# Kernel optimization log

Hardware: AMD Instinct MI355X
Metric: run time of the kernel (lower is better)

## Reference

```python
import jax, jax.numpy as jnp
import numpy as np
import math

DIM = 512
BLOCK_NUM = 16
SEQ_LEN = 8192
BLOCK_LEN = SEQ_LEN // BLOCK_NUM  # 512 == DIM -> mask used as-is
BATCH = 4
LN_EPS = 1e-3  # keras LayerNormalization default epsilon


def setup_inputs() -> dict:
    key = jax.random.key(0)
    ks = jax.random.split(key, 5)
    inputs = jax.random.normal(ks[0], (BATCH, BLOCK_NUM, BLOCK_LEN, DIM), dtype=jnp.float32)
    # binary padding-style mask, values in {0,1}
    mask_array = jax.random.randint(ks[1], (BATCH, SEQ_LEN, DIM), 0, 2).astype(jnp.float32)
    scale = 1.0 / math.sqrt(DIM)
    dw1 = jax.random.normal(ks[2], (DIM, DIM), dtype=jnp.float32) * scale
    dw2 = jax.random.normal(ks[3], (DIM, DIM), dtype=jnp.float32) * scale
    dw3 = jax.random.normal(ks[4], (DIM, DIM), dtype=jnp.float32) * scale
    db1 = jnp.zeros((DIM,), dtype=jnp.float32)
    db2 = jnp.zeros((DIM,), dtype=jnp.float32)
    db3 = jnp.zeros((DIM,), dtype=jnp.float32)
    return {"inputs": inputs, "mask_array": mask_array,
            "dw1": dw1, "dw2": dw2, "dw3": dw3,
            "db1": db1, "db2": db2, "db3": db3}


def reference(inputs, mask_array, dw1, dw2, dw3, db1, db2, db3):
    # inputs: [B, block_num, block_len, dim]
    Q = jnp.matmul(inputs, dw1) + db1
    K = jnp.matmul(inputs, dw2) + db2
    V = jnpp_matmul = jnp.matmul(inputs, dw3) + db3
    V = jnp.matmul(inputs, dw3) + db3
    # block-local attention scores: [B, bn, bl, bl]
    scores = jnp.einsum('bnqd,bnkd->bnqk', Q, K) / math.sqrt(DIM)
    # mask: [B, seq_len, dim] -> [B, bn, bl, dim]; block_len == dim so no slice/tile
    m = mask_array.reshape(BATCH, BLOCK_NUM, BLOCK_LEN, DIM)
    scores = scores + (1.0 - m) * jnp.float32(-1e10)
    p = jax.nn.softmax(scores, axis=-1)
    out = jnp.einsum('bnqk,bnkd->bnqd', p, V) + inputs  # residual
    # LayerNorm(axis=-1), fresh keras layer: gamma=1, beta=0, eps=1e-3
    mean = jnp.mean(out, axis=-1, keepdims=True)
    var = jnp.mean(jnp.square(out - mean), axis=-1, keepdims=True)
    return (out - mean) / jnp.sqrt(var + LN_EPS)
```

## Files before the change

kernel.cpp:

```cpp
#include <hip/hip_runtime.h>

#define DIMK 512
#define NBLK 64
#define NTOK 32768

typedef short  short8 __attribute__((ext_vector_type(8)));
typedef float  f32x4  __attribute__((ext_vector_type(4)));
typedef unsigned short u16x8 __attribute__((ext_vector_type(8)));

__device__ __forceinline__ unsigned short f2bf(float f) {
  union { float f; unsigned u; } v; v.f = f;
  unsigned r = (v.u + 0x7FFFu + ((v.u >> 16) & 1u)) >> 16;
  return (unsigned short)r;
}
__device__ __forceinline__ float bf2f(unsigned short h) {
  return __uint_as_float(((unsigned)h) << 16);
}

__device__ __forceinline__ void gload_lds16(const unsigned short* g,
                                            unsigned short* l) {
  __builtin_amdgcn_global_load_lds(
      (const __attribute__((address_space(1))) unsigned int*)(g),
      (__attribute__((address_space(3))) unsigned int*)(l),
      16, 0, 0);
}


__global__ __launch_bounds__(256) void k_wt_prep(
    const float* __restrict__ dw1, const float* __restrict__ dw2,
    const float* __restrict__ dw3, unsigned short* __restrict__ Wt)
{
  __shared__ float t[64][65];
  const int b = blockIdx.x;
  const int w = b >> 6;
  const int tt = b & 63;
  const int kt = (tt >> 3) * 64;
  const int nt = (tt & 7) * 64;
  const float* dw = (w == 0) ? dw1 : (w == 1) ? dw2 : dw3;
  const int tid = threadIdx.x;
  const int rr = tid >> 4;
  const int cc = (tid & 15) << 2;

#pragma unroll
  for (int p = 0; p < 4; ++p) {
    const int r = rr + p * 16;
    const float4 v = *(const float4*)&dw[(size_t)(kt + r) * 512 + nt + cc];
    t[cc + 0][r] = v.x; t[cc + 1][r] = v.y;
    t[cc + 2][r] = v.z; t[cc + 3][r] = v.w;
  }
  __syncthreads();
#pragma unroll
  for (int p = 0; p < 4; ++p) {
    const int r = rr + p * 16;
    const int n = nt + r;
    const int k = kt + cc;
    ushort4 o;
    o.x = f2bf(t[r][cc + 0]); o.y = f2bf(t[r][cc + 1]);
    o.z = f2bf(t[r][cc + 2]); o.w = f2bf(t[r][cc + 3]);
    *(ushort4*)&Wt[(size_t)w * 262144 + (size_t)(k >> 5) * 16384 +
                   (size_t)n * 32 + (k & 31)] = o;
  }
}

__global__ __launch_bounds__(256) void k_xconv(
    const float* __restrict__ X, unsigned short* __restrict__ Xb)
{
  const size_t gid = (size_t)blockIdx.x * 256 + threadIdx.x;
  const size_t i = gid * 8;
  const int tok = (int)(i >> 9);
  const int col = (int)(i & 511);
  const float4 a = *(const float4*)(X + i);
  const float4 b = *(const float4*)(X + i + 4);
  u16x8 o;
  o[0] = f2bf(a.x); o[1] = f2bf(a.y); o[2] = f2bf(a.z); o[3] = f2bf(a.w);
  o[4] = f2bf(b.x); o[5] = f2bf(b.y); o[6] = f2bf(b.z); o[7] = f2bf(b.w);
  *(u16x8*)(Xb + ((size_t)(tok >> 7) * 16 + (col >> 5)) * 4096 +
            (tok & 127) * 32 + (col & 31)) = o;
}

__global__ __launch_bounds__(256) void k_bitpack(
    const float* __restrict__ mask, unsigned char* __restrict__ bits)
{
  const size_t gid = (size_t)blockIdx.x * 256 + threadIdx.x;
  const size_t i = gid * 8;
  const float4 ma = *(const float4*)(mask + i);
  const float4 mb = *(const float4*)(mask + i + 4);
  unsigned v = 0;
  v |= (ma.x > 0.5f) << 0; v |= (ma.y > 0.5f) << 1;
  v |= (ma.z > 0.5f) << 2; v |= (ma.w > 0.5f) << 3;
  v |= (mb.x > 0.5f) << 4; v |= (mb.y > 0.5f) << 5;
  v |= (mb.z > 0.5f) << 6; v |= (mb.w > 0.5f) << 7;
  bits[gid] = (unsigned char)v;
}

__global__ __launch_bounds__(256, 2) void k_qkv(
    const unsigned short* __restrict__ Xb, const unsigned short* __restrict__ Wt,
    const float* __restrict__ db1, const float* __restrict__ db2,
    const float* __restrict__ db3,
    unsigned short* __restrict__ Qb, unsigned short* __restrict__ Kb,
    unsigned short* __restrict__ Vt)
{
  __shared__ __align__(16) unsigned short smem[32768];

  const int id = blockIdx.x;
  const int x = id & 7, j = id >> 3;
  const int mtile = x * 32 + (j >> 2);
  const int nt = j & 3;
  const int m0 = mtile * 128;
  const int n0 = nt * 128;

  const int tid = threadIdx.x, lane = tid & 63, wv = tid >> 6;
  const int quad = lane >> 4, l16 = lane & 15;
  const int rb = (wv >> 1) * 64, cb = (wv & 1) * 64;

  f32x4 acc[3][4][4];
#pragma unroll
  for (int w = 0; w < 3; ++w)
#pragma unroll
    for (int i = 0; i < 4; ++i)
#pragma unroll
      for (int jj = 0; jj < 4; ++jj) {
        f32x4 z = {0.f, 0.f, 0.f, 0.f}; acc[w][i][jj] = z;
      }

  auto stage = [&](unsigned short* base, int it) {
    const unsigned short* aslab = Xb + ((size_t)mtile * 16 + it) * 4096;
    gload_lds16(aslab + tid * 8, base + tid * 8);
    gload_lds16(aslab + (tid + 256) * 8, base + (tid + 256) * 8);
#pragma unroll
    for (int h = 0; h < 6; ++h) {
      const int c = tid + h * 256;
      const int w = c >> 9, cc = c & 511;
      const unsigned short* bslab =
          Wt + (size_t)w * 262144 + (size_t)it * 16384 + (size_t)n0 * 32;
      gload_lds16(bslab + cc * 8, base + 4096 + w * 4096 + cc * 8);
    }
  };

  stage(smem, 0);
  __syncthreads();
  int cur = 0;
  for (int it = 0; it < 16; ++it) {
    unsigned short* cbuf = smem + cur * 16384;
    if (it < 15) stage(smem + (cur ^ 1) * 16384, it + 1);
    const unsigned short* As = cbuf;
    const unsigned short* Bs = cbuf + 4096;
    short8 af[4];
#pragma unroll
    for (int i = 0; i < 4; ++i)
      af[i] = *(const short8*)&As[(rb + i * 16 + l16) * 32 + quad * 8];
#pragma unroll
    for (int jj = 0; jj < 4; ++jj)
#pragma unroll
      for (int w = 0; w < 3; ++w) {
        const short8 bf =
            *(const short8*)&Bs[w * 4096 + (cb + jj * 16 + l16) * 32 + quad * 8];
#pragma unroll
        for (int i = 0; i < 4; ++i)
          acc[w][i][jj] = __builtin_amdgcn_mfma_f32_16x16x32_bf16(
              af[i], bf, acc[w][i][jj], 0, 0, 0);
      }
    __syncthreads();
    cur ^= 1;
  }

#pragma unroll
  for (int i = 0; i < 4; ++i)
#pragma unroll
    for (int jj = 0; jj < 4; ++jj)
#pragma unroll
      for (int r = 0; r < 4; ++r) {
        const int tok = m0 + rb + i * 16 + quad * 4 + r;
        const int col = n0 + cb + jj * 16 + l16;
        Qb[((size_t)(tok >> 6) * 16 + (col >> 5)) * 2048 +
           (tok & 63) * 32 + (col & 31)] = f2bf(acc[0][i][jj][r] + db1[col]);
        Kb[((size_t)(tok >> 9) * 16 + (col >> 5)) * 16384 +
           (tok & 511) * 32 + (col & 31)] = f2bf(acc[1][i][jj][r] + db2[col]);
      }
#pragma unroll
  for (int i = 0; i < 4; ++i)
#pragma unroll
    for (int jj = 0; jj < 4; ++jj) {
      const int cl = cb + jj * 16 + l16;
      const int t0 = rb + i * 16 + quad * 4;
      const float bv = db3[n0 + cl];
      ushort4 pk;
      pk.x = f2bf(acc[2][i][jj][0] + bv);
      pk.y = f2bf(acc[2][i][jj][1] + bv);
      pk.z = f2bf(acc[2][i][jj][2] + bv);
      pk.w = f2bf(acc[2][i][jj][3] + bv);
      *(ushort4*)&smem[cl * 136 + t0] = pk;
    }
  __syncthreads();
#pragma unroll
  for (int h = 0; h < 8; ++h) {
    const int c = tid + h * 256;
    const int cl = c >> 4, toff = (c & 15) * 8;
    const int tg = mtile * 128 + toff;
    *(u16x8*)&Vt[(size_t)(tg >> 5) * 16384 + (size_t)(n0 + cl) * 32 +
                 (tg & 31)] = *(const u16x8*)&smem[cl * 136 + toff];
  }
}

__global__ __launch_bounds__(256, 2) void k_attn_p(
    const unsigned short* __restrict__ Qb, const unsigned short* __restrict__ Kb,
    const unsigned long long* __restrict__ bits, unsigned short* __restrict__ Pb)
{
  __shared__ __align__(16) unsigned short smem[36864];
  __shared__ float red[4][64];
  const int tid = threadIdx.x, lane = tid & 63, wv = tid >> 6;
  const int quad = lane >> 4, l16 = lane & 15;
  const int blk = blockIdx.x & 63, mt = blockIdx.x >> 6;
  const size_t q0 = (size_t)blk * 512 + (size_t)mt * 64;
  const int qt = blk * 8 + mt;

  f32x4 acc[4][8];
#pragma unroll
  for (int i = 0; i < 4; ++i)
#pragma unroll
    for (int j = 0; j < 8; ++j) { f32x4 z = {0.f, 0.f, 0.f, 0.f}; acc[i][j] = z; }

  auto stage = [&](unsigned short* base, int it) {
    const unsigned short* aslab = Qb + ((size_t)qt * 16 + it) * 2048;
    gload_lds16(aslab + tid * 8, base + tid * 8);
    const unsigned short* bslab = Kb + ((size_t)blk * 16 + it) * 16384;
#pragma unroll
    for (int h = 0; h < 8; ++h) {
      const int c = tid + h * 256;
      gload_lds16(bslab + c * 8, base + 2048 + c * 8);
    }
  };

  stage(smem, 0);
  __syncthreads();
  int cur = 0;
  for (int it = 0; it < 16; ++it) {
    unsigned short* cbuf = smem + cur * 18432;
    if (it < 15) stage(smem + (cur ^ 1) * 18432, it + 1);
    const unsigned short* As = cbuf;
    const unsigned short* Bs = cbuf + 2048;
    short8 af[4], bfv[8];
#pragma unroll
    for (int i = 0; i < 4; ++i)
      af[i] = *(const short8*)&As[(i * 16 + l16) * 32 + quad * 8];
#pragma unroll
    for (int j = 0; j < 8; ++j)
      bfv[j] = *(const short8*)&Bs[(wv * 128 + j * 16 + l16) * 32 + quad * 8];
#pragma unroll
    for (int i = 0; i < 4; ++i)
#pragma unroll
      for (int j = 0; j < 8; ++j)
        acc[i][j] = __builtin_amdgcn_mfma_f32_16x16x32_bf16(
            af[i], bfv[j], acc[i][j], 0, 0, 0);
    __syncthreads();
    cur ^= 1;
  }

  const float scale = 0.04419417382415922f;
  float rmax[4][4];
#pragma unroll
  for (int i = 0; i < 4; ++i)
#pragma unroll
    for (int r = 0; r < 4; ++r) rmax[i][r] = -3.0e38f;
#pragma unroll
  for (int i = 0; i < 4; ++i)
#pragma unroll
    for (int r = 0; r < 4; ++r) {
      const size_t tok = q0 + i * 16 + quad * 4 + r;
      const unsigned long long w0 = bits[tok * 8 + wv * 2];
      const unsigned long long w1 = bits[tok * 8 + wv * 2 + 1];
#pragma unroll
      for (int j = 0; j < 8; ++j) {
        const unsigned long long sel = (j < 4) ? w0 : w1;
        const float bias = ((sel >> (l16 + 16 * (j & 3))) & 1ull) ? 0.0f : -1e10f;
        const float v = acc[i][j][r] * scale + bias;
        acc[i][j][r] = v;
        rmax[i][r] = fmaxf(rmax[i][r], v);
      }
    }
#pragma unroll
  for (int i = 0; i < 4; ++i)
#pragma unroll
    for (int r = 0; r < 4; ++r)
      for (int d = 1; d < 16; d <<= 1)
        rmax[i][r] = fmaxf(rmax[i][r], __shfl_xor(rmax[i][r], d, 64));
  if (l16 == 0)
#pragma unroll
    for (int i = 0; i < 4; ++i)
#pragma unroll
      for (int r = 0; r < 4; ++r) red[wv][i * 16 + quad * 4 + r] = rmax[i][r];
  __syncthreads();
#pragma unroll
  for (int i = 0; i < 4; ++i)
#pragma unroll
    for (int r = 0; r < 4; ++r) {
      const int row = i * 16 + quad * 4 + r;
      rmax[i][r] = fmaxf(fmaxf(red[0][row], red[1][row]),
                         fmaxf(red[2][row], red[3][row]));
    }
  __syncthreads();
  float rsum[4][4];
#pragma unroll
  for (int i = 0; i < 4; ++i)
#pragma unroll
    for (int r = 0; r < 4; ++r) rsum[i][r] = 0.f;
#pragma unroll
  for (int i = 0; i < 4; ++i)
#pragma unroll
    for (int j = 0; j < 8; ++j)
#pragma unroll
      for (int r = 0; r < 4; ++r) {
        const float e = __expf(acc[i][j][r] - rmax[i][r]);
        acc[i][j][r] = e;
        rsum[i][r] += e;
      }
#pragma unroll
  for (int i = 0; i < 4; ++i)
#pragma unroll
    for (int r = 0; r < 4; ++r)
      for (int d = 1; d < 16; d <<= 1)
        rsum[i][r] += __shfl_xor(rsum[i][r], d, 64);
  if (l16 == 0)
#pragma unroll
    for (int i = 0; i < 4; ++i)
#pragma unroll
      for (int r = 0; r < 4; ++r) red[wv][i * 16 + quad * 4 + r] = rsum[i][r];
  __syncthreads();
#pragma unroll
  for (int i = 0; i < 4; ++i)
#pragma unroll
    for (int r = 0; r < 4; ++r) {
      const int row = i * 16 + quad * 4 + r;
      rsum[i][r] = 1.0f / (red[0][row] + red[1][row] + red[2][row] + red[3][row]);
    }
#pragma unroll
  for (int i = 0; i < 4; ++i)
#pragma unroll
    for (int j = 0; j < 8; ++j)
#pragma unroll
      for (int r = 0; r < 4; ++r) {
        const int tok = (int)(q0 + i * 16 + quad * 4 + r);
        const int col = wv * 128 + j * 16 + l16;
        Pb[((size_t)(tok >> 6) * 16 + (col >> 5)) * 2048 +
           (tok & 63) * 32 + (col & 31)] = f2bf(acc[i][j][r] * rsum[i][r]);
      }
}

__global__ __launch_bounds__(256, 2) void k_pv_ln(
    const unsigned short* __restrict__ Pb, const unsigned short* __restrict__ Vt,
    const unsigned short* __restrict__ Xb, float* __restrict__ Out)
{
  __shared__ __align__(16) unsigned short smem[36864];
  __shared__ float2 red[4][64];
  const int tid = threadIdx.x, lane = tid & 63, wv = tid >> 6;
  const int quad = lane >> 4, l16 = lane & 15;
  const int blk = blockIdx.x & 63, mt = blockIdx.x >> 6;
  const size_t q0 = (size_t)blk * 512 + (size_t)mt * 64;
  const int qt = blk * 8 + mt;

  f32x4 acc[4][8];
#pragma unroll
  for (int i = 0; i < 4; ++i)
#pragma unroll
    for (int j = 0; j < 8; ++j) { f32x4 z = {0.f, 0.f, 0.f, 0.f}; acc[i][j] = z; }

  auto stage = [&](unsigned short* base, int it) {
    const unsigned short* aslab = Pb + ((size_t)qt * 16 + it) * 2048;
    gload_lds16(aslab + tid * 8, base + tid * 8);
    const unsigned short* bslab = Vt + ((size_t)blk * 16 + it) * 16384;
#pragma unroll
    for (int h = 0; h < 8; ++h) {
      const int c = tid + h * 256;
      gload_lds16(bslab + c * 8, base + 2048 + c * 8);
    }
  };

  stage(smem, 0);
  __syncthreads();
  int cur = 0;
  for (int it = 0; it < 16; ++it) {
    unsigned short* cbuf = smem + cur * 18432;
    if (it < 15) stage(smem + (cur ^ 1) * 18432, it + 1);
    const unsigned short* As = cbuf;
    const unsigned short* Bs = cbuf + 2048;
    short8 af[4], bfv[8];
#pragma unroll
    for (int i = 0; i < 4; ++i)
      af[i] = *(const short8*)&As[(i * 16 + l16) * 32 + quad * 8];
#pragma unroll
    for (int j = 0; j < 8; ++j)
      bfv[j] = *(const short8*)&Bs[(wv * 128 + j * 16 + l16) * 32 + quad * 8];
#pragma unroll
    for (int i = 0; i < 4; ++i)
#pragma unroll
      for (int j = 0; j < 8; ++j)
        acc[i][j] = __builtin_amdgcn_mfma_f32_16x16x32_bf16(
            af[i], bfv[j], acc[i][j], 0, 0, 0);
    __syncthreads();
    cur ^= 1;
  }

  float vsum[4][4], vsq[4][4];
#pragma unroll
  for (int i = 0; i < 4; ++i)
#pragma unroll
    for (int r = 0; r < 4; ++r) { vsum[i][r] = 0.f; vsq[i][r] = 0.f; }
#pragma unroll
  for (int i = 0; i < 4; ++i)
#pragma unroll
    for (int j = 0; j < 8; ++j)
#pragma unroll
      for (int r = 0; r < 4; ++r) {
        const int tok = (int)(q0 + i * 16 + quad * 4 + r);
        const int col = wv * 128 + j * 16 + l16;
        const float v = acc[i][j][r] +
            bf2f(Xb[((size_t)(tok >> 7) * 16 + (col >> 5)) * 4096 +
                    (tok & 127) * 32 + (col & 31)]);
        acc[i][j][r] = v;
        vsum[i][r] += v;
        vsq[i][r] += v * v;
      }
#pragma unroll
  for (int i = 0; i < 4; ++i)
#pragma unroll
    for (int r = 0; r < 4; ++r)
      for (int d = 1; d < 16; d <<= 1) {
        vsum[i][r] += __shfl_xor(vsum[i][r], d, 64);
        vsq[i][r]  += __shfl_xor(vsq[i][r], d, 64);
      }
  if (l16 == 0)
#pragma unroll
    for (int i = 0; i < 4; ++i)
#pragma unroll
      for (int r = 0; r < 4; ++r) {
        float2 p; p.x = vsum[i][r]; p.y = vsq[i][r];
        red[wv][i * 16 + quad * 4 + r] = p;
      }
  __syncthreads();
#pragma unroll
  for (int i = 0; i < 4; ++i)
#pragma unroll
    for (int r = 0; r < 4; ++r) {
      const int row = i * 16 + quad * 4 + r;
      float s = 0.f, q = 0.f;
#pragma unroll
      for (int w = 0; w < 4; ++w) { s += red[w][row].x; q += red[w][row].y; }
      const float mean = s * (1.0f / 512.0f);
      const float var  = q * (1.0f / 512.0f) - mean * mean;
      vsum[i][r] = mean;
      vsq[i][r]  = rsqrtf(var + 1e-3f);
    }
#pragma unroll
  for (int i = 0; i < 4; ++i)
#pragma unroll
    for (int j = 0; j < 8; ++j)
#pragma unroll
      for (int r = 0; r < 4; ++r) {
        const size_t tok = q0 + i * 16 + quad * 4 + r;
        const int col = wv * 128 + j * 16 + l16;
        Out[tok * (size_t)DIMK + col] =
            (acc[i][j][r] - vsum[i][r]) * vsq[i][r];
      }
}

extern "C" void kernel_launch(void* const* d_in, const int* in_sizes, int n_in,
                              void* d_out, int out_size, void* d_ws, size_t ws_size,
                              hipStream_t stream)
{
  const float* X    = (const float*)d_in[0];
  const float* mask = (const float*)d_in[1];
  const float* dw1  = (const float*)d_in[2];
  const float* dw2  = (const float*)d_in[3];
  const float* dw3  = (const float*)d_in[4];
  const float* db1  = (const float*)d_in[5];
  const float* db2  = (const float*)d_in[6];
  const float* db3  = (const float*)d_in[7];
  float* Out = (float*)d_out;

  char* ws = (char*)d_ws;
  const size_t MB = 1ull << 20;
  unsigned short* Wt = (unsigned short*)(ws);
  unsigned short* Qb = (unsigned short*)(ws + 2 * MB);
  unsigned short* Kb = (unsigned short*)(ws + 34 * MB);
  unsigned short* Vt = (unsigned short*)(ws + 66 * MB);
  unsigned short* Xb = (unsigned short*)(ws + 98 * MB);
  unsigned short* Pb = Qb;
  unsigned char*  bits = (unsigned char*)d_out;

  k_wt_prep<<<192, 256, 0, stream>>>(dw1, dw2, dw3, Wt);
  k_xconv  <<<8192, 256, 0, stream>>>(X, Xb);
  k_bitpack<<<8192, 256, 0, stream>>>(mask, bits);
  k_qkv    <<<1024, 256, 0, stream>>>(Xb, Wt, db1, db2, db3, Qb, Kb, Vt);
  k_attn_p <<<512, 256, 0, stream>>>(Qb, Kb, (const unsigned long long*)bits, Pb);
  k_pv_ln  <<<512, 256, 0, stream>>>(Pb, Vt, Xb, Out);
}
```

Baseline: 302.8 us.

## Triple-buffer GEMM loops, swizzle LDS layout, and merge prep kernels

The three GEMM-style kernels move from double to triple buffering. Each iteration now waits with an explicit vmcnt so loads run two stages ahead and the per-iteration __syncthreads calls are gone. The global-to-LDS copies use an XOR swizzle on 16-byte chunks, with matching swizzled fragment reads, to cut LDS bank conflicts. Launch bounds drop to one block per CU to make room for the larger LDS footprint, and the three preprocessing kernels are merged into one launch. The larger LDS use lowers occupancy, and the hard-coded vmcnt values depend on how many loads each stage issues.

```diff
diff --git a/kernel.cpp b/kernel.cpp
--- a/kernel.cpp
+++ b/kernel.cpp
@@ -25,82 +25,81 @@
       16, 0, 0);
 }
 
-
-__global__ __launch_bounds__(256) void k_wt_prep(
+__device__ __forceinline__ int swz(int c) { return c ^ ((c >> 3) & 3); }
+
+
+__global__ __launch_bounds__(256) void k_prep(
+    const float* __restrict__ X, const float* __restrict__ mask,
     const float* __restrict__ dw1, const float* __restrict__ dw2,
-    const float* __restrict__ dw3, unsigned short* __restrict__ Wt)
+    const float* __restrict__ dw3,
+    unsigned short* __restrict__ Xb, unsigned char* __restrict__ bits,
+    unsigned short* __restrict__ Wt)
 {
   __shared__ float t[64][65];
   const int b = blockIdx.x;
-  const int w = b >> 6;
-  const int tt = b & 63;
-  const int kt = (tt >> 3) * 64;
-  const int nt = (tt & 7) * 64;
-  const float* dw = (w == 0) ? dw1 : (w == 1) ? dw2 : dw3;
   const int tid = threadIdx.x;
-  const int rr = tid >> 4;
-  const int cc = (tid & 15) << 2;
-
-#pragma unroll
-  for (int p = 0; p < 4; ++p) {
-    const int r = rr + p * 16;
-    const float4 v = *(const float4*)&dw[(size_t)(kt + r) * 512 + nt + cc];
-    t[cc + 0][r] = v.x; t[cc + 1][r] = v.y;
-    t[cc + 2][r] = v.z; t[cc + 3][r] = v.w;
+  if (b < 8192) {
+    const size_t gid = (size_t)b * 256 + tid;
+    const size_t i = gid * 8;
+    const int tok = (int)(i >> 9);
+    const int col = (int)(i & 511);
+    const float4 a = *(const float4*)(X + i);
+    const float4 bb = *(const float4*)(X + i + 4);
+    u16x8 o;
+    o[0] = f2bf(a.x); o[1] = f2bf(a.y); o[2] = f2bf(a.z); o[3] = f2bf(a.w);
+    o[4] = f2bf(bb.x); o[5] = f2bf(bb.y); o[6] = f2bf(bb.z); o[7] = f2bf(bb.w);
+    *(u16x8*)(Xb + ((size_t)(tok >> 7) * 16 + (col >> 5)) * 4096 +
+              (tok & 127) * 32 + (col & 31)) = o;
+  } else if (b < 16384) {
+    const size_t gid = (size_t)(b - 8192) * 256 + tid;
+    const size_t i = gid * 8;
+    const float4 ma = *(const float4*)(mask + i);
+    const float4 mb = *(const float4*)(mask + i + 4);
+    unsigned v = 0;
+    v |= (ma.x > 0.5f) << 0; v |= (ma.y > 0.5f) << 1;
+    v |= (ma.z > 0.5f) << 2; v |= (ma.w > 0.5f) << 3;
+    v |= (mb.x > 0.5f) << 4; v |= (mb.y > 0.5f) << 5;
+    v |= (mb.z > 0.5f) << 6; v |= (mb.w > 0.5f) << 7;
+    bits[gid] = (unsigned char)v;
+  } else {
+    const int bb = b - 16384;
+    const int w = bb >> 6;
+    const int tt = bb & 63;
+    const int kt = (tt >> 3) * 64;
+    const int nt = (tt & 7) * 64;
+    const float* dw = (w == 0) ? dw1 : (w == 1) ? dw2 : dw3;
+    const int rr = tid >> 4;
+    const int cc = (tid & 15) << 2;
+#pragma unroll
+    for (int p = 0; p < 4; ++p) {
+      const int r = rr + p * 16;
+      const float4 v = *(const float4*)&dw[(size_t)(kt + r) * 512 + nt + cc];
+      t[cc + 0][r] = v.x; t[cc + 1][r] = v.y;
+      t[cc + 2][r] = v.z; t[cc + 3][r] = v.w;
+    }
+    __syncthreads();
+#pragma unroll
+    for (int p = 0; p < 4; ++p) {
+      const int r = rr + p * 16;
+      const int n = nt + r;
+      const int k = kt + cc;
+      ushort4 o;
+      o.x = f2bf(t[r][cc + 0]); o.y = f2bf(t[r][cc + 1]);
+      o.z = f2bf(t[r][cc + 2]); o.w = f2bf(t[r][cc + 3]);
+      *(ushort4*)&Wt[(size_t)w * 262144 + (size_t)(k >> 5) * 16384 +
+                     (size_t)n * 32 + (k & 31)] = o;
+    }
   }
-  __syncthreads();
-#pragma unroll
-  for (int p = 0; p < 4; ++p) {
-    const int r = rr + p * 16;
-    const int n = nt + r;
-    const int k = kt + cc;
-    ushort4 o;
-    o.x = f2bf(t[r][cc + 0]); o.y = f2bf(t[r][cc + 1]);
-    o.z = f2bf(t[r][cc + 2]); o.w = f2bf(t[r][cc + 3]);
-    *(ushort4*)&Wt[(size_t)w * 262144 + (size_t)(k >> 5) * 16384 +
-                   (size_t)n * 32 + (k & 31)] = o;
-  }
-}
-
-__global__ __launch_bounds__(256) void k_xconv(
-    const float* __restrict__ X, unsigned short* __restrict__ Xb)
-{
-  const size_t gid = (size_t)blockIdx.x * 256 + threadIdx.x;
-  const size_t i = gid * 8;
-  const int tok = (int)(i >> 9);
-  const int col = (int)(i & 511);
-  const float4 a = *(const float4*)(X + i);
-  const float4 b = *(const float4*)(X + i + 4);
-  u16x8 o;
-  o[0] = f2bf(a.x); o[1] = f2bf(a.y); o[2] = f2bf(a.z); o[3] = f2bf(a.w);
-  o[4] = f2bf(b.x); o[5] = f2bf(b.y); o[6] = f2bf(b.z); o[7] = f2bf(b.w);
-  *(u16x8*)(Xb + ((size_t)(tok >> 7) * 16 + (col >> 5)) * 4096 +
-            (tok & 127) * 32 + (col & 31)) = o;
-}
-
-__global__ __launch_bounds__(256) void k_bitpack(
-    const float* __restrict__ mask, unsigned char* __restrict__ bits)
-{
-  const size_t gid = (size_t)blockIdx.x * 256 + threadIdx.x;
-  const size_t i = gid * 8;
-  const float4 ma = *(const float4*)(mask + i);
-  const float4 mb = *(const float4*)(mask + i + 4);
-  unsigned v = 0;
-  v |= (ma.x > 0.5f) << 0; v |= (ma.y > 0.5f) << 1;
-  v |= (ma.z > 0.5f) << 2; v |= (ma.w > 0.5f) << 3;
-  v |= (mb.x > 0.5f) << 4; v |= (mb.y > 0.5f) << 5;
-  v |= (mb.z > 0.5f) << 6; v |= (mb.w > 0.5f) << 7;
-  bits[gid] = (unsigned char)v;
-}
-
-__global__ __launch_bounds__(256, 2) void k_qkv(
+}
+
+__global__ __launch_bounds__(256, 1) void k_qkv(
     const unsigned short* __restrict__ Xb, const unsigned short* __restrict__ Wt,
     const float* __restrict__ db1, const float* __restrict__ db2,
     const float* __restrict__ db3,
     unsigned short* __restrict__ Qb, unsigned short* __restrict__ Kb,
     unsigned short* __restrict__ Vt)
 {
-  __shared__ __align__(16) unsigned short smem[32768];
+  __shared__ __align__(16) unsigned short smem[49152];
 
   const int id = blockIdx.x;
   const int x = id & 7, j = id >> 3;
@@ -111,6 +110,7 @@
 
   const int tid = threadIdx.x, lane = tid & 63, wv = tid >> 6;
   const int quad = lane >> 4, l16 = lane & 15;
+  const int qx = quad ^ ((l16 >> 1) & 3);
   const int rb = (wv >> 1) * 64, cb = (wv & 1) * 64;
 
   f32x4 acc[3][4][4];
@@ -123,46 +123,48 @@
         f32x4 z = {0.f, 0.f, 0.f, 0.f}; acc[w][i][jj] = z;
       }
 
-  auto stage = [&](unsigned short* base, int it) {
+  auto stage = [&](int it) {
+    unsigned short* base = smem + (it % 3) * 16384;
     const unsigned short* aslab = Xb + ((size_t)mtile * 16 + it) * 4096;
-    gload_lds16(aslab + tid * 8, base + tid * 8);
-    gload_lds16(aslab + (tid + 256) * 8, base + (tid + 256) * 8);
+    gload_lds16(aslab + swz(tid) * 8, base + tid * 8);
+    gload_lds16(aslab + swz(tid + 256) * 8, base + (tid + 256) * 8);
 #pragma unroll
     for (int h = 0; h < 6; ++h) {
       const int c = tid + h * 256;
       const int w = c >> 9, cc = c & 511;
       const unsigned short* bslab =
           Wt + (size_t)w * 262144 + (size_t)it * 16384 + (size_t)n0 * 32;
-      gload_lds16(bslab + cc * 8, base + 4096 + w * 4096 + cc * 8);
+      gload_lds16(bslab + swz(cc) * 8, base + 4096 + w * 4096 + cc * 8);
     }
   };
 
-  stage(smem, 0);
-  __syncthreads();
-  int cur = 0;
+  stage(0);
+  stage(1);
   for (int it = 0; it < 16; ++it) {
-    unsigned short* cbuf = smem + cur * 16384;
-    if (it < 15) stage(smem + (cur ^ 1) * 16384, it + 1);
-    const unsigned short* As = cbuf;
-    const unsigned short* Bs = cbuf + 4096;
+    if (it < 15) asm volatile("s_waitcnt vmcnt(8)" ::: "memory");
+    else         asm volatile("s_waitcnt vmcnt(0)" ::: "memory");
+    __builtin_amdgcn_s_barrier();
+    __builtin_amdgcn_sched_barrier(0);
+    if (it + 2 < 16) stage(it + 2);
+    const unsigned short* As = smem + (it % 3) * 16384;
+    const unsigned short* Bs = As + 4096;
     short8 af[4];
 #pragma unroll
     for (int i = 0; i < 4; ++i)
-      af[i] = *(const short8*)&As[(rb + i * 16 + l16) * 32 + quad * 8];
+      af[i] = *(const short8*)&As[(rb + i * 16 + l16) * 32 + qx * 8];
 #pragma unroll
     for (int jj = 0; jj < 4; ++jj)
 #pragma unroll
       for (int w = 0; w < 3; ++w) {
         const short8 bf =
-            *(const short8*)&Bs[w * 4096 + (cb + jj * 16 + l16) * 32 + quad * 8];
+            *(const short8*)&Bs[w * 4096 + (cb + jj * 16 + l16) * 32 + qx * 8];
 #pragma unroll
         for (int i = 0; i < 4; ++i)
           acc[w][i][jj] = __builtin_amdgcn_mfma_f32_16x16x32_bf16(
               af[i], bf, acc[w][i][jj], 0, 0, 0);
       }
-    __syncthreads();
-    cur ^= 1;
   }
+  __syncthreads();
 
 #pragma unroll
   for (int i = 0; i < 4; ++i)
@@ -202,14 +204,15 @@
   }
 }
 
-__global__ __launch_bounds__(256, 2) void k_attn_p(
+__global__ __launch_bounds__(256, 1) void k_attn_p(
     const unsigned short* __restrict__ Qb, const unsigned short* __restrict__ Kb,
     const unsigned long long* __restrict__ bits, unsigned short* __restrict__ Pb)
 {
-  __shared__ __align__(16) unsigned short smem[36864];
+  __shared__ __align__(16) unsigned short smem[55296];
   __shared__ float red[4][64];
   const int tid = threadIdx.x, lane = tid & 63, wv = tid >> 6;
   const int quad = lane >> 4, l16 = lane & 15;
+  const int qx = quad ^ ((l16 >> 1) & 3);
   const int blk = blockIdx.x & 63, mt = blockIdx.x >> 6;
   const size_t q0 = (size_t)blk * 512 + (size_t)mt * 64;
   const int qt = blk * 8 + mt;
@@ -220,40 +223,41 @@
 #pragma unroll
     for (int j = 0; j < 8; ++j) { f32x4 z = {0.f, 0.f, 0.f, 0.f}; acc[i][j] = z; }
 
-  auto stage = [&](unsigned short* base, int it) {
+  auto stage = [&](int it) {
+    unsigned short* base = smem + (it % 3) * 18432;
     const unsigned short* aslab = Qb + ((size_t)qt * 16 + it) * 2048;
-    gload_lds16(aslab + tid * 8, base + tid * 8);
+    gload_lds16(aslab + swz(tid) * 8, base + tid * 8);
     const unsigned short* bslab = Kb + ((size_t)blk * 16 + it) * 16384;
 #pragma unroll
     for (int h = 0; h < 8; ++h) {
       const int c = tid + h * 256;
-      gload_lds16(bslab + c * 8, base + 2048 + c * 8);
+      gload_lds16(bslab + swz(c) * 8, base + 2048 + c * 8);
     }
   };
 
-  stage(smem, 0);
-  __syncthreads();
-  int cur = 0;
+  stage(0);
+  stage(1);
   for (int it = 0; it < 16; ++it) {
-    unsigned short* cbuf = smem + cur * 18432;
-    if (it < 15) stage(smem + (cur ^ 1) * 18432, it + 1);
-    const unsigned short* As = cbuf;
-    const unsigned short* Bs = cbuf + 2048;
+    if (it < 15) asm volatile("s_waitcnt vmcnt(9)" ::: "memory");
+    else         asm volatile("s_waitcnt vmcnt(0)" ::: "memory");
+    __builtin_amdgcn_s_barrier();
+    __builtin_amdgcn_sched_barrier(0);
+    if (it + 2 < 16) stage(it + 2);
+    const unsigned short* As = smem + (it % 3) * 18432;
+    const unsigned short* Bs = As + 2048;
     short8 af[4], bfv[8];
 #pragma unroll
     for (int i = 0; i < 4; ++i)
-      af[i] = *(const short8*)&As[(i * 16 + l16) * 32 + quad * 8];
+      af[i] = *(const short8*)&As[(i * 16 + l16) * 32 + qx * 8];
 #pragma unroll
     for (int j = 0; j < 8; ++j)
-      bfv[j] = *(const short8*)&Bs[(wv * 128 + j * 16 + l16) * 32 + quad * 8];
+      bfv[j] = *(const short8*)&Bs[(wv * 128 + j * 16 + l16) * 32 + qx * 8];
 #pragma unroll
     for (int i = 0; i < 4; ++i)
 #pragma unroll
       for (int j = 0; j < 8; ++j)
         acc[i][j] = __builtin_amdgcn_mfma_f32_16x16x32_bf16(
             af[i], bfv[j], acc[i][j], 0, 0, 0);
-    __syncthreads();
-    cur ^= 1;
   }
 
   const float scale = 0.04419417382415922f;
@@ -346,14 +350,15 @@
       }
 }
 
-__global__ __launch_bounds__(256, 2) void k_pv_ln(
+__global__ __launch_bounds__(256, 1) void k_pv_ln(
     const unsigned short* __restrict__ Pb, const unsigned short* __restrict__ Vt,
     const unsigned short* __restrict__ Xb, float* __restrict__ Out)
 {
-  __shared__ __align__(16) unsigned short smem[36864];
+  __shared__ __align__(16) unsigned short smem[55296];
   __shared__ float2 red[4][64];
   const int tid = threadIdx.x, lane = tid & 63, wv = tid >> 6;
   const int quad = lane >> 4, l16 = lane & 15;
+  const int qx = quad ^ ((l16 >> 1) & 3);
   const int blk = blockIdx.x & 63, mt = blockIdx.x >> 6;
   const size_t q0 = (size_t)blk * 512 + (size_t)mt * 64;
   const int qt = blk * 8 + mt;
@@ -364,40 +369,41 @@
 #pragma unroll
     for (int j = 0; j < 8; ++j) { f32x4 z = {0.f, 0.f, 0.f, 0.f}; acc[i][j] = z; }
 
-  auto stage = [&](unsigned short* base, int it) {
+  auto stage = [&](int it) {
+    unsigned short* base = smem + (it % 3) * 18432;
     const unsigned short* aslab = Pb + ((size_t)qt * 16 + it) * 2048;
-    gload_lds16(aslab + tid * 8, base + tid * 8);
+    gload_lds16(aslab + swz(tid) * 8, base + tid * 8);
     const unsigned short* bslab = Vt + ((size_t)blk * 16 + it) * 16384;
 #pragma unroll
     for (int h = 0; h < 8; ++h) {
       const int c = tid + h * 256;
-      gload_lds16(bslab + c * 8, base + 2048 + c * 8);
+      gload_lds16(bslab + swz(c) * 8, base + 2048 + c * 8);
     }
   };
 
-  stage(smem, 0);
-  __syncthreads();
-  int cur = 0;
+  stage(0);
+  stage(1);
   for (int it = 0; it < 16; ++it) {
-    unsigned short* cbuf = smem + cur * 18432;
-    if (it < 15) stage(smem + (cur ^ 1) * 18432, it + 1);
-    const unsigned short* As = cbuf;
-    const unsigned short* Bs = cbuf + 2048;
+    if (it < 15) asm volatile("s_waitcnt vmcnt(9)" ::: "memory");
+    else         asm volatile("s_waitcnt vmcnt(0)" ::: "memory");
+    __builtin_amdgcn_s_barrier();
+    __builtin_amdgcn_sched_barrier(0);
+    if (it + 2 < 16) stage(it + 2);
+    const unsigned short* As = smem + (it % 3) * 18432;
+    const unsigned short* Bs = As + 2048;
     short8 af[4], bfv[8];
 #pragma unroll
     for (int i = 0; i < 4; ++i)
-      af[i] = *(const short8*)&As[(i * 16 + l16) * 32 + quad * 8];
+      af[i] = *(const short8*)&As[(i * 16 + l16) * 32 + qx * 8];
 #pragma unroll
     for (int j = 0; j < 8; ++j)
-      bfv[j] = *(const short8*)&Bs[(wv * 128 + j * 16 + l16) * 32 + quad * 8];
+      bfv[j] = *(const short8*)&Bs[(wv * 128 + j * 16 + l16) * 32 + qx * 8];
 #pragma unroll
     for (int i = 0; i < 4; ++i)
 #pragma unroll
       for (int j = 0; j < 8; ++j)
         acc[i][j] = __builtin_amdgcn_mfma_f32_16x16x32_bf16(
             af[i], bfv[j], acc[i][j], 0, 0, 0);
-    __syncthreads();
-    cur ^= 1;
   }
 
   float vsum[4][4], vsq[4][4];
@@ -487,9 +493,7 @@
   unsigned short* Pb = Qb;
   unsigned char*  bits = (unsigned char*)d_out;
 
-  k_wt_prep<<<192, 256, 0, stream>>>(dw1, dw2, dw3, Wt);
-  k_xconv  <<<8192, 256, 0, stream>>>(X, Xb);
-  k_bitpack<<<8192, 256, 0, stream>>>(mask, bits);
+  k_prep   <<<16576, 256, 0, stream>>>(X, mask, dw1, dw2, dw3, Xb, bits, Wt);
   k_qkv    <<<1024, 256, 0, stream>>>(Xb, Wt, db1, db2, db3, Qb, Kb, Vt);
   k_attn_p <<<512, 256, 0, stream>>>(Qb, Kb, (const unsigned long long*)bits, Pb);
   k_pv_ln  <<<512, 256, 0, stream>>>(Pb, Vt, Xb, Out);
```

Result: slower. 346.0 us (+14.3%).
